# Kernel optimization log

Hardware: AMD Instinct MI355X
Metric: run time of the kernel (lower is better)

The kernel has to match this reference:

```python
import jax, jax.numpy as jnp
import numpy as np

B, TM1, N, H = 512, 256, 128, 64  # batch, T-1, input_size, hidden_size


def setup_inputs() -> dict:
    key = jax.random.key(0)
    ks = jax.random.split(key, 7)
    s = 0.05
    return {
        "input_data": jax.random.normal(ks[0], (B, TM1, N), dtype=jnp.float32),
        "attn_w": jax.random.normal(ks[1], (1, 2 * H + TM1), dtype=jnp.float32) * s,
        "attn_b": jax.random.normal(ks[2], (1,), dtype=jnp.float32) * s,
        "W_ih": jax.random.normal(ks[3], (4 * H, N), dtype=jnp.float32) * s,
        "W_hh": jax.random.normal(ks[4], (4 * H, H), dtype=jnp.float32) * s,
        "b_ih": jax.random.normal(ks[5], (4 * H,), dtype=jnp.float32) * s,
        "b_hh": jax.random.normal(ks[6], (4 * H,), dtype=jnp.float32) * s,
    }


def reference(input_data, attn_w, attn_b, W_ih, W_hh, b_ih, b_hh):
    b, tm1, n = input_data.shape
    h_dim = W_hh.shape[1]
    # (B, N, T-1): each driving series over the full window, used every step
    x_series = jnp.transpose(input_data, (0, 2, 1))
    aw = attn_w[0]  # (2H + T-1,)
    ab = attn_b[0]

    def step(carry, x_t):  # x_t: (B, N) inputs at time t
        h, c = carry  # (B, H) each
        # attention scores: concat(h, c, x_series) @ aw, done without materializing concat
        s_hc = h @ aw[:h_dim] + c @ aw[h_dim:2 * h_dim]  # (B,)
        s_x = x_series @ aw[2 * h_dim:]  # (B, N)
        a = jax.nn.softmax(s_x + s_hc[:, None] + ab, axis=1)  # softmax over driving series
        wx = a * x_t  # (B, N) weighted input
        # single LSTM cell step (PyTorch gate order i, f, g, o)
        gates = wx @ W_ih.T + b_ih + h @ W_hh.T + b_hh  # (B, 4H)
        i, f, g, o = jnp.split(gates, 4, axis=1)
        c2 = jax.nn.sigmoid(f) * c + jax.nn.sigmoid(i) * jnp.tanh(g)
        h2 = jax.nn.sigmoid(o) * jnp.tanh(c2)
        return (h2, c2), (wx, h2)

    h0 = jnp.zeros((b, h_dim), dtype=input_data.dtype)
    c0 = jnp.zeros((b, h_dim), dtype=input_data.dtype)
    xs = jnp.transpose(input_data, (1, 0, 2))  # (T-1, B, N)
    _, (wxs, hs) = jax.lax.scan(step, (h0, c0), xs)
    input_weighted = jnp.transpose(wxs, (1, 0, 2))  # (B, T-1, N)
    input_encoded = jnp.transpose(hs, (1, 0, 2))  # (B, T-1, H)
    return input_weighted, input_encoded
```

## Files before the change

kernel.cpp:

```cpp
#include <hip/hip_runtime.h>
#include <hip/hip_fp16.h>
#include <cstdint>
#include <cstddef>

#define B_ 512
#define T_ 256
#define N_ 128
#define H_ 64
#define G_ 256

typedef __attribute__((ext_vector_type(8))) short short8;
typedef __attribute__((ext_vector_type(4))) float f32x4;
typedef _Float16 half2_t __attribute__((ext_vector_type(2)));

static __device__ __forceinline__ unsigned short f2bf(float f) {
    union { float f; unsigned int i; } v;
    v.f = f;
    unsigned int x = v.i;
    return (unsigned short)((x + 0x7fffu + ((x >> 16) & 1u)) >> 16);
}
static __device__ __forceinline__ half2_t u2h2(unsigned int u) {
    union { unsigned int u; half2_t h; } v; v.u = u; return v.h;
}
static __device__ __forceinline__ unsigned int h2u(half2_t h) {
    union { half2_t h; unsigned int u; } v; v.h = h; return v.u;
}

__global__ __launch_bounds__(256) void k_awgemm(const float* __restrict__ x,
                                                const float* __restrict__ attn_w,
                                                const float* __restrict__ W_ih,
                                                const float* __restrict__ b_ih,
                                                const float* __restrict__ b_hh,
                                                float* __restrict__ iw,
                                                _Float16* __restrict__ gatesx) {
    __shared__ __align__(16) unsigned short Wl[G_][136];
    __shared__ __align__(16) unsigned short Al[32][136];
    __shared__ float bias[G_];
    __shared__ float aw_s[T_];
    __shared__ float a_s[N_];
    __shared__ float wred[4];
    const int tid = threadIdx.x;
    const int b = blockIdx.x;

    for (int q = tid; q < G_ * 32; q += 256) {
        int r = q >> 5, c4 = (q & 31) << 2;
        float4 v = *(const float4*)(W_ih + r * N_ + c4);
        Wl[r][c4 + 0] = f2bf(v.x); Wl[r][c4 + 1] = f2bf(v.y);
        Wl[r][c4 + 2] = f2bf(v.z); Wl[r][c4 + 3] = f2bf(v.w);
    }
    bias[tid] = b_ih[tid] + b_hh[tid];
    aw_s[tid] = attn_w[2 * H_ + tid];
    __syncthreads();

    float (*red)[128] = (float(*)[128])&Al[0][0];
    const int n0 = (tid & 31) << 2;
    const int tg = tid >> 5;
    const float* xb = x + (size_t)b * (T_ * N_);
    {
        float p0 = 0.f, p1 = 0.f, p2 = 0.f, p3 = 0.f;
        for (int t = tg; t < T_; t += 8) {
            float4 v = *(const float4*)(xb + t * N_ + n0);
            float w = aw_s[t];
            p0 += v.x * w; p1 += v.y * w; p2 += v.z * w; p3 += v.w * w;
        }
        red[tg][n0 + 0] = p0; red[tg][n0 + 1] = p1;
        red[tg][n0 + 2] = p2; red[tg][n0 + 3] = p3;
    }
    __syncthreads();
    {
        float s = 0.f;
        if (tid < 128) {
            #pragma unroll
            for (int g = 0; g < 8; ++g) s += red[g][tid];
        }
        float m = (tid < 128) ? s : -1e30f;
        #pragma unroll
        for (int d = 1; d < 64; d <<= 1) m = fmaxf(m, __shfl_xor(m, d));
        if ((tid & 63) == 0) wred[tid >> 6] = m;
        __syncthreads();
        m = fmaxf(wred[0], wred[1]);
        __syncthreads();
        float e = (tid < 128) ? __expf(s - m) : 0.f;
        float z = e;
        #pragma unroll
        for (int d = 1; d < 64; d <<= 1) z += __shfl_xor(z, d);
        if ((tid & 63) == 0) wred[tid >> 6] = z;
        __syncthreads();
        z = wred[0] + wred[1];
        if (tid < 128) a_s[tid] = e / z;
    }
    __syncthreads();

    const int lane = tid & 63;
    const int lr = lane & 15;
    const int lk = (lane >> 4) << 3;
    const int gc0 = (tid >> 6) << 6;
    const int orow = (lane >> 4) << 2;

    for (int st = 0; st < 8; ++st) {
        const int r0 = b * T_ + st * 32;
        __syncthreads();
        for (int q = tid; q < 32 * 32; q += 256) {
            int r = q >> 5, c4 = (q & 31) << 2;
            size_t off = (size_t)(r0 + r) * N_ + c4;
            float4 v = *(const float4*)(x + off);
            float4 w;
            w.x = a_s[c4 + 0] * v.x; w.y = a_s[c4 + 1] * v.y;
            w.z = a_s[c4 + 2] * v.z; w.w = a_s[c4 + 3] * v.w;
            *(float4*)(iw + off) = w;
            Al[r][c4 + 0] = f2bf(w.x); Al[r][c4 + 1] = f2bf(w.y);
            Al[r][c4 + 2] = f2bf(w.z); Al[r][c4 + 3] = f2bf(w.w);
        }
        __syncthreads();

        f32x4 acc[2][4];
        #pragma unroll
        for (int mt = 0; mt < 2; ++mt)
            #pragma unroll
            for (int nt = 0; nt < 4; ++nt)
                acc[mt][nt] = (f32x4){0.f, 0.f, 0.f, 0.f};

        #pragma unroll
        for (int kk = 0; kk < N_; kk += 32) {
            short8 af0 = *(const short8*)(&Al[lr][kk + lk]);
            short8 af1 = *(const short8*)(&Al[16 + lr][kk + lk]);
            #pragma unroll
            for (int nt = 0; nt < 4; ++nt) {
                short8 bfv = *(const short8*)(&Wl[gc0 + nt * 16 + lr][kk + lk]);
                acc[0][nt] = __builtin_amdgcn_mfma_f32_16x16x32_bf16(af0, bfv, acc[0][nt], 0, 0, 0);
                acc[1][nt] = __builtin_amdgcn_mfma_f32_16x16x32_bf16(af1, bfv, acc[1][nt], 0, 0, 0);
            }
        }
        #pragma unroll
        for (int mt = 0; mt < 2; ++mt) {
            #pragma unroll
            for (int nt = 0; nt < 4; ++nt) {
                int col = gc0 + nt * 16 + lr;
                float bs = bias[col];
                #pragma unroll
                for (int rg = 0; rg < 4; ++rg) {
                    int rr = r0 + mt * 16 + orow + rg;
                    gatesx[(size_t)rr * G_ + col] = (_Float16)(acc[mt][nt][rg] + bs);
                }
            }
        }
    }
}

__global__ __attribute__((amdgpu_flat_work_group_size(256, 256)))
__attribute__((amdgpu_waves_per_eu(2, 4)))
void k_rnn3(const _Float16* __restrict__ gatesx,
            const float* __restrict__ W_hh,
            float* __restrict__ enc) {
    __shared__ __align__(16) _Float16 hb[H_];
    __shared__ float act[G_];
    const int tid = threadIdx.x;
    const int b = blockIdx.x;
    const int wv = tid >> 6;

    half2_t w2[32];
    #pragma unroll
    for (int q = 0; q < 8; ++q) {
        float4 v0 = *(const float4*)(W_hh + tid * H_ + q * 8);
        float4 v1 = *(const float4*)(W_hh + tid * H_ + q * 8 + 4);
        w2[4 * q + 0] = (half2_t){(_Float16)v0.x, (_Float16)v0.y};
        w2[4 * q + 1] = (half2_t){(_Float16)v0.z, (_Float16)v0.w};
        w2[4 * q + 2] = (half2_t){(_Float16)v1.x, (_Float16)v1.y};
        w2[4 * q + 3] = (half2_t){(_Float16)v1.z, (_Float16)v1.w};
    }
    #pragma unroll
    for (int k = 0; k < 32; ++k) {
        unsigned int u = h2u(w2[k]);
        asm volatile("" : "+v"(u));
        w2[k] = u2h2(u);
    }

    if (tid < 32) ((unsigned int*)hb)[tid] = 0u;
    float c = 0.f;

    const _Float16* gx = gatesx + (size_t)b * T_ * G_ + tid;
    float gcur = (float)gx[0];
    __syncthreads();

    for (int t = 0; t < T_; ++t) {
        _Float16 gn = gx[(size_t)(t + 1 < T_ ? t + 1 : t) * G_];

        float acc = gcur;
        const uint4* hv = (const uint4*)hb;
        #pragma unroll
        for (int q = 0; q < 8; ++q) {
            uint4 ch = hv[q];
            acc = __builtin_amdgcn_fdot2(w2[4 * q + 0], u2h2(ch.x), acc, false);
            acc = __builtin_amdgcn_fdot2(w2[4 * q + 1], u2h2(ch.y), acc, false);
            acc = __builtin_amdgcn_fdot2(w2[4 * q + 2], u2h2(ch.z), acc, false);
            acc = __builtin_amdgcn_fdot2(w2[4 * q + 3], u2h2(ch.w), acc, false);
        }
        float a;
        if (wv == 2) a = 1.f - 2.f / (__expf(2.f * acc) + 1.f);
        else         a = 1.f / (1.f + __expf(-acc));
        act[tid] = a;
        __syncthreads();

        if (tid < H_) {
            float ai = act[tid], af = act[H_ + tid], ag = act[2 * H_ + tid], ao = act[3 * H_ + tid];
            c = af * c + ai * ag;
            float tc = 1.f - 2.f / (__expf(2.f * c) + 1.f);
            float h = ao * tc;
            hb[tid] = (_Float16)h;
            enc[((size_t)b * T_ + t) * H_ + tid] = h;
        }
        __syncthreads();
        gcur = (float)gn;
    }
}

extern "C" void kernel_launch(void* const* d_in, const int* in_sizes, int n_in,
                              void* d_out, int out_size, void* d_ws, size_t ws_size,
                              hipStream_t stream) {
    if (n_in < 7 || in_sizes[0] != B_ * T_ * N_) return;

    const float* x    = (const float*)d_in[0];
    const float* aw   = (const float*)d_in[1];
    const float* W_ih = (const float*)d_in[3];
    const float* W_hh = (const float*)d_in[4];
    const float* b_ih = (const float*)d_in[5];
    const float* b_hh = (const float*)d_in[6];

    float* iwp = (float*)d_out;
    float* enc = (float*)d_out + (size_t)B_ * T_ * N_;

    _Float16* gatesx = (_Float16*)d_ws;
    size_t need = (size_t)B_ * T_ * G_ * sizeof(_Float16);
    if (ws_size < need) return;

    hipLaunchKernelGGL(k_awgemm, dim3(B_), dim3(256), 0, stream,
                       x, aw, W_ih, b_ih, b_hh, iwp, gatesx);
    hipLaunchKernelGGL(k_rnn3, dim3(B_), dim3(256), 0, stream, gatesx, W_hh, enc);
}
```

Measured before the change: 185.2 us.

## Use one wave per batch in recurrence and cache x as bf16 in LDS

The recurrent kernel now uses a single 64-thread wave per batch row. Each lane computes all four gate dot products for its hidden unit, so the act buffer and both per-step block barriers go away and the wave's own lock-step ordering replaces them. The attention/GEMM kernel keeps a bf16 copy of the batch's x window in LDS during the score pass, so the later weighting pass does not re-read x from global memory. In exchange, LDS use rises to about 144KB per block, and the fp32 input_weighted output is now computed from bf16-rounded x, which loses precision.

```diff
diff --git a/kernel.cpp b/kernel.cpp
--- a/kernel.cpp
+++ b/kernel.cpp
@@ -13,6 +13,11 @@
 typedef __attribute__((ext_vector_type(4))) float f32x4;
 typedef _Float16 half2_t __attribute__((ext_vector_type(2)));
 
+static __device__ __forceinline__ float bf2f(unsigned short u) {
+    union { unsigned int i; float f; } v;
+    v.i = ((unsigned int)u) << 16;
+    return v.f;
+}
 static __device__ __forceinline__ unsigned short f2bf(float f) {
     union { float f; unsigned int i; } v;
     v.f = f;
@@ -34,6 +39,7 @@
                                                 float* __restrict__ iw,
                                                 _Float16* __restrict__ gatesx) {
     __shared__ __align__(16) unsigned short Wl[G_][136];
+    __shared__ __align__(16) unsigned short Xl[T_][N_];
     __shared__ __align__(16) unsigned short Al[32][136];
     __shared__ float bias[G_];
     __shared__ float aw_s[T_];
@@ -62,6 +68,8 @@
             float4 v = *(const float4*)(xb + t * N_ + n0);
             float w = aw_s[t];
             p0 += v.x * w; p1 += v.y * w; p2 += v.z * w; p3 += v.w * w;
+            Xl[t][n0 + 0] = f2bf(v.x); Xl[t][n0 + 1] = f2bf(v.y);
+            Xl[t][n0 + 2] = f2bf(v.z); Xl[t][n0 + 3] = f2bf(v.w);
         }
         red[tg][n0 + 0] = p0; red[tg][n0 + 1] = p1;
         red[tg][n0 + 2] = p2; red[tg][n0 + 3] = p3;
@@ -102,12 +110,11 @@
         __syncthreads();
         for (int q = tid; q < 32 * 32; q += 256) {
             int r = q >> 5, c4 = (q & 31) << 2;
-            size_t off = (size_t)(r0 + r) * N_ + c4;
-            float4 v = *(const float4*)(x + off);
+            ushort4 xv = *(const ushort4*)(&Xl[st * 32 + r][c4]);
             float4 w;
-            w.x = a_s[c4 + 0] * v.x; w.y = a_s[c4 + 1] * v.y;
-            w.z = a_s[c4 + 2] * v.z; w.w = a_s[c4 + 3] * v.w;
-            *(float4*)(iw + off) = w;
+            w.x = a_s[c4 + 0] * bf2f(xv.x); w.y = a_s[c4 + 1] * bf2f(xv.y);
+            w.z = a_s[c4 + 2] * bf2f(xv.z); w.w = a_s[c4 + 3] * bf2f(xv.w);
+            *(float4*)(iw + (size_t)(r0 + r) * N_ + c4) = w;
             Al[r][c4 + 0] = f2bf(w.x); Al[r][c4 + 1] = f2bf(w.y);
             Al[r][c4 + 2] = f2bf(w.z); Al[r][c4 + 3] = f2bf(w.w);
         }
@@ -147,70 +154,84 @@
     }
 }
 
-__global__ __attribute__((amdgpu_flat_work_group_size(256, 256)))
-__attribute__((amdgpu_waves_per_eu(2, 4)))
-void k_rnn3(const _Float16* __restrict__ gatesx,
+__global__ __attribute__((amdgpu_flat_work_group_size(64, 64)))
+__attribute__((amdgpu_waves_per_eu(1, 2)))
+void k_rnn4(const _Float16* __restrict__ gatesx,
             const float* __restrict__ W_hh,
             float* __restrict__ enc) {
     __shared__ __align__(16) _Float16 hb[H_];
-    __shared__ float act[G_];
-    const int tid = threadIdx.x;
+    const int j = threadIdx.x;
     const int b = blockIdx.x;
-    const int wv = tid >> 6;
-
-    half2_t w2[32];
+
+    half2_t w2[4][32];
     #pragma unroll
-    for (int q = 0; q < 8; ++q) {
-        float4 v0 = *(const float4*)(W_hh + tid * H_ + q * 8);
-        float4 v1 = *(const float4*)(W_hh + tid * H_ + q * 8 + 4);
-        w2[4 * q + 0] = (half2_t){(_Float16)v0.x, (_Float16)v0.y};
-        w2[4 * q + 1] = (half2_t){(_Float16)v0.z, (_Float16)v0.w};
-        w2[4 * q + 2] = (half2_t){(_Float16)v1.x, (_Float16)v1.y};
-        w2[4 * q + 3] = (half2_t){(_Float16)v1.z, (_Float16)v1.w};
+    for (int g = 0; g < 4; ++g) {
+        const float* src = W_hh + (size_t)(g * H_ + j) * H_;
+        #pragma unroll
+        for (int q = 0; q < 16; ++q) {
+            float4 v = *(const float4*)(src + q * 4);
+            w2[g][2 * q + 0] = (half2_t){(_Float16)v.x, (_Float16)v.y};
+            w2[g][2 * q + 1] = (half2_t){(_Float16)v.z, (_Float16)v.w};
+        }
     }
     #pragma unroll
-    for (int k = 0; k < 32; ++k) {
-        unsigned int u = h2u(w2[k]);
-        asm volatile("" : "+v"(u));
-        w2[k] = u2h2(u);
-    }
-
-    if (tid < 32) ((unsigned int*)hb)[tid] = 0u;
+    for (int g = 0; g < 4; ++g) {
+        #pragma unroll
+        for (int k = 0; k < 32; ++k) {
+            unsigned int u = h2u(w2[g][k]);
+            asm volatile("" : "+v"(u));
+            w2[g][k] = u2h2(u);
+        }
+    }
+
+    if (j < 32) ((unsigned int*)hb)[j] = 0u;
+    __syncthreads();
     float c = 0.f;
 
-    const _Float16* gx = gatesx + (size_t)b * T_ * G_ + tid;
-    float gcur = (float)gx[0];
-    __syncthreads();
+    const _Float16* gx = gatesx + (size_t)b * T_ * G_ + j;
+    float g0 = (float)gx[0];
+    float g1 = (float)gx[64];
+    float g2 = (float)gx[128];
+    float g3 = (float)gx[192];
 
     for (int t = 0; t < T_; ++t) {
-        _Float16 gn = gx[(size_t)(t + 1 < T_ ? t + 1 : t) * G_];
-
-        float acc = gcur;
+        const _Float16* gp = gx + (size_t)(t + 1 < T_ ? t + 1 : t) * G_;
+        _Float16 n0 = gp[0], n1 = gp[64], n2 = gp[128], n3 = gp[192];
+
         const uint4* hv = (const uint4*)hb;
+        float a0 = g0, a1 = g1, a2 = g2, a3 = g3;
         #pragma unroll
         for (int q = 0; q < 8; ++q) {
             uint4 ch = hv[q];
-            acc = __builtin_amdgcn_fdot2(w2[4 * q + 0], u2h2(ch.x), acc, false);
-            acc = __builtin_amdgcn_fdot2(w2[4 * q + 1], u2h2(ch.y), acc, false);
-            acc = __builtin_amdgcn_fdot2(w2[4 * q + 2], u2h2(ch.z), acc, false);
-            acc = __builtin_amdgcn_fdot2(w2[4 * q + 3], u2h2(ch.w), acc, false);
-        }
-        float a;
-        if (wv == 2) a = 1.f - 2.f / (__expf(2.f * acc) + 1.f);
-        else         a = 1.f / (1.f + __expf(-acc));
-        act[tid] = a;
-        __syncthreads();
-
-        if (tid < H_) {
-            float ai = act[tid], af = act[H_ + tid], ag = act[2 * H_ + tid], ao = act[3 * H_ + tid];
-            c = af * c + ai * ag;
-            float tc = 1.f - 2.f / (__expf(2.f * c) + 1.f);
-            float h = ao * tc;
-            hb[tid] = (_Float16)h;
-            enc[((size_t)b * T_ + t) * H_ + tid] = h;
-        }
-        __syncthreads();
-        gcur = (float)gn;
+            a0 = __builtin_amdgcn_fdot2(w2[0][4 * q + 0], u2h2(ch.x), a0, false);
+            a1 = __builtin_amdgcn_fdot2(w2[1][4 * q + 0], u2h2(ch.x), a1, false);
+            a2 = __builtin_amdgcn_fdot2(w2[2][4 * q + 0], u2h2(ch.x), a2, false);
+            a3 = __builtin_amdgcn_fdot2(w2[3][4 * q + 0], u2h2(ch.x), a3, false);
+            a0 = __builtin_amdgcn_fdot2(w2[0][4 * q + 1], u2h2(ch.y), a0, false);
+            a1 = __builtin_amdgcn_fdot2(w2[1][4 * q + 1], u2h2(ch.y), a1, false);
+            a2 = __builtin_amdgcn_fdot2(w2[2][4 * q + 1], u2h2(ch.y), a2, false);
+            a3 = __builtin_amdgcn_fdot2(w2[3][4 * q + 1], u2h2(ch.y), a3, false);
+            a0 = __builtin_amdgcn_fdot2(w2[0][4 * q + 2], u2h2(ch.z), a0, false);
+            a1 = __builtin_amdgcn_fdot2(w2[1][4 * q + 2], u2h2(ch.z), a1, false);
+            a2 = __builtin_amdgcn_fdot2(w2[2][4 * q + 2], u2h2(ch.z), a2, false);
+            a3 = __builtin_amdgcn_fdot2(w2[3][4 * q + 2], u2h2(ch.z), a3, false);
+            a0 = __builtin_amdgcn_fdot2(w2[0][4 * q + 3], u2h2(ch.w), a0, false);
+            a1 = __builtin_amdgcn_fdot2(w2[1][4 * q + 3], u2h2(ch.w), a1, false);
+            a2 = __builtin_amdgcn_fdot2(w2[2][4 * q + 3], u2h2(ch.w), a2, false);
+            a3 = __builtin_amdgcn_fdot2(w2[3][4 * q + 3], u2h2(ch.w), a3, false);
+        }
+
+        float si = 1.f / (1.f + __expf(-a0));
+        float sf = 1.f / (1.f + __expf(-a1));
+        float tg = 1.f - 2.f / (__expf(2.f * a2) + 1.f);
+        float so = 1.f / (1.f + __expf(-a3));
+        c = sf * c + si * tg;
+        float tc = 1.f - 2.f / (__expf(2.f * c) + 1.f);
+        float h = so * tc;
+
+        hb[j] = (_Float16)h;
+        enc[((size_t)b * T_ + t) * H_ + j] = h;
+        g0 = (float)n0; g1 = (float)n1; g2 = (float)n2; g3 = (float)n3;
     }
 }
 
@@ -235,5 +256,5 @@
 
     hipLaunchKernelGGL(k_awgemm, dim3(B_), dim3(256), 0, stream,
                        x, aw, W_ih, b_ih, b_hh, iwp, gatesx);
-    hipLaunchKernelGGL(k_rnn3, dim3(B_), dim3(256), 0, stream, gatesx, W_hh, enc);
-}
+    hipLaunchKernelGGL(k_rnn4, dim3(B_), dim3(64), 0, stream, gatesx, W_hh, enc);
+}
```

Result: slower. 219.4 us (+18.5%).
